# Performance work log

Hardware: AMD Instinct MI355X
Metric: run time of the kernel (lower is better)

Reference implementation:

```python
import jax, jax.numpy as jnp
import numpy as np

D = 1024
B = 16384

def setup_inputs() -> dict:
    key = jax.random.key(0)
    ks = jax.random.split(key, 8)
    s = 1.0 / np.sqrt(D)  # torch Linear default init scale (uniform), use scaled normal
    return {
        "f1": jax.random.normal(ks[0], (B, D), jnp.float32),
        "f2": jax.random.normal(ks[1], (B, D), jnp.float32),
        "Wq": jax.random.normal(ks[2], (D, D), jnp.float32) * s,
        "bq": jax.random.normal(ks[3], (D,), jnp.float32) * s,
        "Wk": jax.random.normal(ks[4], (D, D), jnp.float32) * s,
        "bk": jax.random.normal(ks[5], (D,), jnp.float32) * s,
        "Wv": jax.random.normal(ks[6], (D, D), jnp.float32) * s,
        "bv": jax.random.normal(ks[7], (D,), jnp.float32) * s,
    }

def reference(f1, f2, Wq, bq, Wk, bk, Wv, bv):
    d = f1.shape[-1]
    feats = jnp.stack([f1, f2], axis=1)          # [B, 2, D]
    # nn.Linear: y = x @ W.T + b
    Q = jnp.einsum("bsd,ed->bse", feats, Wq) + bq  # [B, 2, D]
    K = jnp.einsum("bsd,ed->bse", feats, Wk) + bk
    V = jnp.einsum("bsd,ed->bse", feats, Wv) + bv
    scores = jnp.einsum("bse,bte->bst", Q, K) / jnp.sqrt(jnp.asarray(d, feats.dtype))  # [B, 2, 2]
    attn = jax.nn.softmax(scores, axis=-1)
    attended = jnp.einsum("bst,btd->bsd", attn, V)  # [B, 2, D]
    return attended.sum(axis=1)                     # [B, D]
```

## Files before the change

kernel.cpp:

```cpp
#include <hip/hip_runtime.h>
#include <hip/hip_bf16.h>
#include <stdint.h>

typedef unsigned short u16;
typedef __bf16 bf16x8 __attribute__((ext_vector_type(8)));
typedef float f32x4 __attribute__((ext_vector_type(4)));

#define D_DIM 1024
#define B_ROWS 16384
#define M_ROWS 32768
#define BM 128
#define BN 128
#define BK 64

__device__ __forceinline__ u16 f2bs(float f) {
    union { float f; unsigned u; } v; v.f = f;
    unsigned r = v.u + 0x7FFFu + ((v.u >> 16) & 1u);
    return (u16)(r >> 16);
}
__device__ __forceinline__ float bs2f(unsigned bits16) {
    union { unsigned u; float f; } v; v.u = bits16 << 16;
    return v.f;
}
__device__ __forceinline__ float bidx(uint2 v, int e) {
    unsigned w = (e < 2) ? v.x : v.y;
    unsigned sh = (unsigned)(e & 1) * 16u;
    return bs2f((w >> sh) & 0xFFFFu);
}
__device__ __forceinline__ uint2 pack4(float4 f) {
    uint2 r;
    r.x = (unsigned)f2bs(f.x) | ((unsigned)f2bs(f.y) << 16);
    r.y = (unsigned)f2bs(f.z) | ((unsigned)f2bs(f.w) << 16);
    return r;
}

#define GLD16(gsrc, ldst)                                                      \
    __builtin_amdgcn_global_load_lds(                                          \
        (const __attribute__((address_space(1))) void*)(gsrc),                 \
        (__attribute__((address_space(3))) void*)(ldst), 16, 0, 0)

__global__ __launch_bounds__(256) void cvt_feats(const float* __restrict__ f1,
                                                 const float* __restrict__ f2,
                                                 u16* __restrict__ X) {
    size_t i4   = (size_t)blockIdx.x * 256 + threadIdx.x;
    size_t base = i4 * 4;
    size_t brow = base >> 10;
    size_t col  = base & 1023;
    float4 a = *(const float4*)(f1 + base);
    float4 b = *(const float4*)(f2 + base);
    *(uint2*)(X + (2 * brow) * D_DIM + col)     = pack4(a);
    *(uint2*)(X + (2 * brow + 1) * D_DIM + col) = pack4(b);
}

__global__ __launch_bounds__(256) void cvt_wv(const float* __restrict__ Wv,
                                              u16* __restrict__ Wvb) {
    size_t base = ((size_t)blockIdx.x * 256 + threadIdx.x) * 4;
    *(uint2*)(Wvb + base) = pack4(*(const float4*)(Wv + base));
}

__global__ __launch_bounds__(256) void transpose_bf16(const float* __restrict__ in,
                                                      u16* __restrict__ out) {
    __shared__ float lds[32][33];
    const int tx = threadIdx.x & 31;
    const int ty = threadIdx.x >> 5;
    const int r0 = (blockIdx.x >> 5) * 32;
    const int c0 = (blockIdx.x & 31) * 32;
#pragma unroll
    for (int i = 0; i < 4; ++i) {
        int r = ty + i * 8;
        lds[r][tx] = in[(size_t)(r0 + r) * D_DIM + c0 + tx];
    }
    __syncthreads();
#pragma unroll
    for (int i = 0; i < 4; ++i) {
        int r = ty + i * 8;
        out[(size_t)(c0 + r) * D_DIM + r0 + tx] = f2bs(lds[tx][r]);
    }
}

__global__ __launch_bounds__(256) void uvc_k(const float* __restrict__ Wq,
                                             const float* __restrict__ Wk,
                                             const float* __restrict__ bq,
                                             const float* __restrict__ bk,
                                             float* __restrict__ u,
                                             float* __restrict__ v,
                                             float* __restrict__ cbuf) {
    const int dl = threadIdx.x & 31;
    const int fg = threadIdx.x >> 5;
    const int d  = blockIdx.x * 32 + dl;
    float au = 0.f, av = 0.f;
    const int f0 = fg * 128;
    for (int f = f0; f < f0 + 128; ++f) {
        au = fmaf(Wq[(size_t)f * D_DIM + d], bk[f], au);
        av = fmaf(Wk[(size_t)f * D_DIM + d], bq[f], av);
    }
    __shared__ float su[8][32], sv[8][32];
    su[fg][dl] = au; sv[fg][dl] = av;
    __syncthreads();
    if (fg == 0) {
        float a = 0.f, b2 = 0.f;
#pragma unroll
        for (int g = 0; g < 8; ++g) { a += su[g][dl]; b2 += sv[g][dl]; }
        u[d] = a; v[d] = b2;
    }
    if (blockIdx.x == 0) {
        __shared__ float red[256];
        float p = 0.f;
        for (int f = threadIdx.x; f < D_DIM; f += 256) p = fmaf(bq[f], bk[f], p);
        red[threadIdx.x] = p;
        __syncthreads();
        for (int s = 128; s; s >>= 1) {
            if (threadIdx.x < s) red[threadIdx.x] += red[threadIdx.x + s];
            __syncthreads();
        }
        if (threadIdx.x == 0) cbuf[0] = red[0];
    }
}

__global__ __launch_bounds__(256, 3) void gemm_bt(const u16* __restrict__ A,
                                                  const u16* __restrict__ W,
                                                  const float* __restrict__ bias,
                                                  u16* __restrict__ C, int ncols) {
    constexpr int K = D_DIM;
    __shared__ u16 As[BM * BK];
    __shared__ u16 Bs[BN * BK];

    const int cpx  = gridDim.x >> 3;
    const int orig = (blockIdx.x & 7) * cpx + (blockIdx.x >> 3);
    const int nTn = ncols / BN;
    const int m0 = (orig / nTn) * BM, n0 = (orig % nTn) * BN;

    const int tid  = threadIdx.x;
    const int lane = tid & 63;
    const int wave = tid >> 6;
    const int wr = wave >> 1, wc = wave & 1;

    const int lr = lane & 15;
    const int kg = lane >> 4;

    f32x4 acc[4][4] = {};

    const int sr  = tid >> 3;
    const int scs = ((tid & 7) ^ ((tid >> 3) & 7)) * 8;
    const u16* aRow = A + (size_t)(m0 + sr) * K + scs;
    const u16* bRow = W + (size_t)(n0 + sr) * K + scs;
    u16* aDst = As + tid * 8;
    u16* bDst = Bs + tid * 8;

    for (int kt = 0; kt < K; kt += BK) {
#pragma unroll
        for (int i = 0; i < 4; ++i) {
            GLD16(aRow + (size_t)i * 32 * K + kt, aDst + i * 2048);
            GLD16(bRow + (size_t)i * 32 * K + kt, bDst + i * 2048);
        }
        __syncthreads();

#pragma unroll
        for (int kk = 0; kk < 2; ++kk) {
            bf16x8 af[4], bfr[4];
            const int kx = kk * 4 + kg;
#pragma unroll
            for (int mf = 0; mf < 4; ++mf) {
                const int R = wr * 64 + mf * 16 + lr;
                af[mf] = *(const bf16x8*)(As + R * 64 + ((kx ^ (R & 7)) * 8));
            }
#pragma unroll
            for (int nf = 0; nf < 4; ++nf) {
                const int S = wc * 64 + nf * 16 + lr;
                bfr[nf] = *(const bf16x8*)(Bs + S * 64 + ((kx ^ (S & 7)) * 8));
            }
#pragma unroll
            for (int mf = 0; mf < 4; ++mf)
#pragma unroll
                for (int nf = 0; nf < 4; ++nf)
                    acc[mf][nf] = __builtin_amdgcn_mfma_f32_16x16x32_bf16(
                        af[mf], bfr[nf], acc[mf][nf], 0, 0, 0);
        }
        __syncthreads();
    }

    const int cr = (lane >> 4) * 4;
    const int cc = lane & 15;
#pragma unroll
    for (int mf = 0; mf < 4; ++mf) {
#pragma unroll
        for (int nf = 0; nf < 4; ++nf) {
            int col = n0 + wc * 64 + nf * 16 + cc;
            float bsv = bias ? bias[col] : 0.f;
#pragma unroll
            for (int j = 0; j < 4; ++j) {
                int row = m0 + wr * 64 + mf * 16 + cr + j;
                C[(size_t)row * ncols + col] = f2bs(acc[mf][nf][j] + bsv);
            }
        }
    }
}

__global__ __launch_bounds__(256, 3) void gemm_cmb(const u16* __restrict__ A,
                                                   const u16* __restrict__ W,
                                                   const float* __restrict__ bias,
                                                   const float2* __restrict__ wts,
                                                   float* __restrict__ out) {
    constexpr int K = D_DIM;
    constexpr int ncols = D_DIM;
    __shared__ u16 As[BM * BK];
    __shared__ u16 Bs[BN * BK];

    const int cpx  = gridDim.x >> 3;
    const int orig = (blockIdx.x & 7) * cpx + (blockIdx.x >> 3);
    const int nTn = ncols / BN;
    const int m0 = (orig / nTn) * BM, n0 = (orig % nTn) * BN;

    const int tid  = threadIdx.x;
    const int lane = tid & 63;
    const int wave = tid >> 6;
    const int wr = wave >> 1, wc = wave & 1;

    const int lr = lane & 15;
    const int kg = lane >> 4;

    f32x4 acc[4][4] = {};

    const int sr  = tid >> 3;
    const int scs = ((tid & 7) ^ ((tid >> 3) & 7)) * 8;
    const u16* aRow = A + (size_t)(m0 + sr) * K + scs;
    const u16* bRow = W + (size_t)(n0 + sr) * K + scs;
    u16* aDst = As + tid * 8;
    u16* bDst = Bs + tid * 8;

    for (int kt = 0; kt < K; kt += BK) {
#pragma unroll
        for (int i = 0; i < 4; ++i) {
            GLD16(aRow + (size_t)i * 32 * K + kt, aDst + i * 2048);
            GLD16(bRow + (size_t)i * 32 * K + kt, bDst + i * 2048);
        }
        __syncthreads();

#pragma unroll
        for (int kk = 0; kk < 2; ++kk) {
            bf16x8 af[4], bfr[4];
            const int kx = kk * 4 + kg;
#pragma unroll
            for (int mf = 0; mf < 4; ++mf) {
                const int R = wr * 64 + mf * 16 + lr;
                af[mf] = *(const bf16x8*)(As + R * 64 + ((kx ^ (R & 7)) * 8));
            }
#pragma unroll
            for (int nf = 0; nf < 4; ++nf) {
                const int S = wc * 64 + nf * 16 + lr;
                bfr[nf] = *(const bf16x8*)(Bs + S * 64 + ((kx ^ (S & 7)) * 8));
            }
#pragma unroll
            for (int mf = 0; mf < 4; ++mf)
#pragma unroll
                for (int nf = 0; nf < 4; ++nf)
                    acc[mf][nf] = __builtin_amdgcn_mfma_f32_16x16x32_bf16(
                        af[mf], bfr[nf], acc[mf][nf], 0, 0, 0);
        }
        __syncthreads();
    }

    const int cr = (lane >> 4) * 4;
    const int cc = lane & 15;
#pragma unroll
    for (int mf = 0; mf < 4; ++mf) {
        const int rowbase = m0 + wr * 64 + mf * 16 + cr;
        const int p0 = rowbase >> 1;
        const float2 w0 = wts[p0];
        const float2 w1 = wts[p0 + 1];
#pragma unroll
        for (int nf = 0; nf < 4; ++nf) {
            int col = n0 + wc * 64 + nf * 16 + cc;
            float bsv = bias[col];
            float o0 = w0.x * (acc[mf][nf][0] + bsv) + w0.y * (acc[mf][nf][1] + bsv);
            float o1 = w1.x * (acc[mf][nf][2] + bsv) + w1.y * (acc[mf][nf][3] + bsv);
            out[(size_t)p0 * D_DIM + col]       = o0;
            out[(size_t)(p0 + 1) * D_DIM + col] = o1;
        }
    }
}

__global__ __launch_bounds__(256) void scores2(const u16* __restrict__ X,
                                               const u16* __restrict__ G,
                                               const float* __restrict__ u,
                                               const float* __restrict__ v,
                                               const float* __restrict__ cbuf,
                                               float2* __restrict__ wts) {
    const int wave = threadIdx.x >> 6;
    const int lane = threadIdx.x & 63;
    const size_t b = (size_t)blockIdx.x * 4 + wave;
    const u16* x0p = X + (2 * b) * D_DIM;
    const u16* x1p = x0p + D_DIM;
    const u16* g0p = G + (2 * b) * D_DIM;
    const u16* g1p = g0p + D_DIM;

    float d00 = 0.f, d01 = 0.f, d10 = 0.f, d11 = 0.f;
    float au0 = 0.f, au1 = 0.f, bv0 = 0.f, bv1 = 0.f;
#pragma unroll
    for (int s = 0; s < 4; ++s) {
        int c = s * 256 + lane * 4;
        uint2 x0 = *(const uint2*)(x0p + c);
        uint2 x1 = *(const uint2*)(x1p + c);
        uint2 g0 = *(const uint2*)(g0p + c);
        uint2 g1 = *(const uint2*)(g1p + c);
        float4 uu = *(const float4*)(u + c);
        float4 vv = *(const float4*)(v + c);
        float uA[4] = {uu.x, uu.y, uu.z, uu.w};
        float vA[4] = {vv.x, vv.y, vv.z, vv.w};
#pragma unroll
        for (int e = 0; e < 4; ++e) {
            float a0 = bidx(x0, e), a1 = bidx(x1, e);
            float c0 = bidx(g0, e), c1 = bidx(g1, e);
            d00 = fmaf(a0, c0, d00); d01 = fmaf(a0, c1, d01);
            d10 = fmaf(a1, c0, d10); d11 = fmaf(a1, c1, d11);
            au0 = fmaf(uA[e], a0, au0); au1 = fmaf(uA[e], a1, au1);
            bv0 = fmaf(vA[e], a0, bv0); bv1 = fmaf(vA[e], a1, bv1);
        }
    }
#pragma unroll
    for (int off = 32; off; off >>= 1) {
        d00 += __shfl_xor(d00, off); d01 += __shfl_xor(d01, off);
        d10 += __shfl_xor(d10, off); d11 += __shfl_xor(d11, off);
        au0 += __shfl_xor(au0, off); au1 += __shfl_xor(au1, off);
        bv0 += __shfl_xor(bv0, off); bv1 += __shfl_xor(bv1, off);
    }
    if (lane == 0) {
        const float cc0 = cbuf[0];
        const float sc = 1.0f / 32.0f;
        float s00 = (d00 + au0 + bv0 + cc0) * sc;
        float s01 = (d01 + au0 + bv1 + cc0) * sc;
        float s10 = (d10 + au1 + bv0 + cc0) * sc;
        float s11 = (d11 + au1 + bv1 + cc0) * sc;
        float mA = fmaxf(s00, s01);
        float e00 = expf(s00 - mA), e01 = expf(s01 - mA);
        float rA = 1.0f / (e00 + e01);
        float mB = fmaxf(s10, s11);
        float e10 = expf(s10 - mB), e11 = expf(s11 - mB);
        float rB = 1.0f / (e10 + e11);
        float2 w;
        w.x = e00 * rA + e10 * rB;
        w.y = e01 * rA + e11 * rB;
        wts[b] = w;
    }
}

extern "C" void kernel_launch(void* const* d_in, const int* in_sizes, int n_in,
                              void* d_out, int out_size, void* d_ws, size_t ws_size,
                              hipStream_t stream) {
    const float* f1 = (const float*)d_in[0];
    const float* f2 = (const float*)d_in[1];
    const float* Wq = (const float*)d_in[2];
    const float* bq = (const float*)d_in[3];
    const float* Wk = (const float*)d_in[4];
    const float* bk = (const float*)d_in[5];
    const float* Wv = (const float*)d_in[6];
    const float* bv = (const float*)d_in[7];
    float* out = (float*)d_out;

    char*   w    = (char*)d_ws;
    u16*    X    = (u16*)w;
    u16*    G    = X + (size_t)M_ROWS * D_DIM;
    u16*    Wvb  = G + (size_t)M_ROWS * D_DIM;
    u16*    WqT  = Wvb + (size_t)D_DIM * D_DIM;
    u16*    WkT  = WqT + (size_t)D_DIM * D_DIM;
    u16*    Mb   = WkT + (size_t)D_DIM * D_DIM;
    float*  u    = (float*)(Mb + (size_t)D_DIM * D_DIM);
    float*  v    = u + D_DIM;
    float*  cbuf = v + D_DIM;
    float2* wts  = (float2*)(cbuf + 64);

    cvt_feats<<<(B_ROWS * D_DIM / 4) / 256, 256, 0, stream>>>(f1, f2, X);
    cvt_wv<<<(D_DIM * D_DIM / 4) / 256, 256, 0, stream>>>(Wv, Wvb);
    transpose_bf16<<<1024, 256, 0, stream>>>(Wq, WqT);
    transpose_bf16<<<1024, 256, 0, stream>>>(Wk, WkT);
    uvc_k<<<D_DIM / 32, 256, 0, stream>>>(Wq, Wk, bq, bk, u, v, cbuf);

    gemm_bt<<<(D_DIM / BM) * (D_DIM / BN), 256, 0, stream>>>(WqT, WkT, nullptr, Mb, D_DIM);
    gemm_bt<<<(M_ROWS / BM) * (D_DIM / BN), 256, 0, stream>>>(X, Mb, nullptr, G, D_DIM);
    scores2<<<B_ROWS / 4, 256, 0, stream>>>(X, G, u, v, cbuf, wts);
    gemm_cmb<<<(M_ROWS / BM) * (D_DIM / BN), 256, 0, stream>>>(X, Wvb, bv, wts, out);
}
```

Before: 234.5 us.

## Double-buffer LDS tiles in both GEMM kernels to overlap loads with MFMA

Both GEMM kernels now keep two LDS buffers for the A and B tiles. They prefetch the next K-tile with direct global-to-LDS loads while MFMAs run on the current tile, and they drop the trailing barrier. This is meant to hide global load latency behind compute. In exchange LDS per block doubles and launch bounds fall from 3 to 2 blocks per CU, which lowers occupancy. A full vmcnt(0) wait is still taken at the top of each iteration.

```diff
diff --git a/kernel.cpp b/kernel.cpp
--- a/kernel.cpp
+++ b/kernel.cpp
@@ -117,13 +117,14 @@
     }
 }
 
-__global__ __launch_bounds__(256, 3) void gemm_bt(const u16* __restrict__ A,
+__global__ __launch_bounds__(256, 2) void gemm_bt(const u16* __restrict__ A,
                                                   const u16* __restrict__ W,
                                                   const float* __restrict__ bias,
                                                   u16* __restrict__ C, int ncols) {
     constexpr int K = D_DIM;
-    __shared__ u16 As[BM * BK];
-    __shared__ u16 Bs[BN * BK];
+    constexpr int TB = BM * BK;
+    __shared__ u16 As[2 * TB];
+    __shared__ u16 Bs[2 * TB];
 
     const int cpx  = gridDim.x >> 3;
     const int orig = (blockIdx.x & 7) * cpx + (blockIdx.x >> 3);
@@ -144,17 +145,27 @@
     const int scs = ((tid & 7) ^ ((tid >> 3) & 7)) * 8;
     const u16* aRow = A + (size_t)(m0 + sr) * K + scs;
     const u16* bRow = W + (size_t)(n0 + sr) * K + scs;
-    u16* aDst = As + tid * 8;
-    u16* bDst = Bs + tid * 8;
-
+
+#define STAGE_AB(p, kt)                                                        \
+    {                                                                          \
+        u16* aD = As + (p) * TB + tid * 8;                                     \
+        u16* bD = Bs + (p) * TB + tid * 8;                                     \
+        _Pragma("unroll")                                                      \
+        for (int i = 0; i < 4; ++i) {                                          \
+            GLD16(aRow + (size_t)i * 32 * K + (kt), aD + i * 2048);            \
+            GLD16(bRow + (size_t)i * 32 * K + (kt), bD + i * 2048);            \
+        }                                                                      \
+    }
+
+    STAGE_AB(0, 0);
+    int cur = 0;
     for (int kt = 0; kt < K; kt += BK) {
-#pragma unroll
-        for (int i = 0; i < 4; ++i) {
-            GLD16(aRow + (size_t)i * 32 * K + kt, aDst + i * 2048);
-            GLD16(bRow + (size_t)i * 32 * K + kt, bDst + i * 2048);
-        }
-        __syncthreads();
-
+        asm volatile("s_waitcnt vmcnt(0)" ::: "memory");
+        __builtin_amdgcn_s_barrier();
+        if (kt + BK < K) STAGE_AB(cur ^ 1, kt + BK);
+
+        const u16* Ab = As + cur * TB;
+        const u16* Bb = Bs + cur * TB;
 #pragma unroll
         for (int kk = 0; kk < 2; ++kk) {
             bf16x8 af[4], bfr[4];
@@ -162,12 +173,12 @@
 #pragma unroll
             for (int mf = 0; mf < 4; ++mf) {
                 const int R = wr * 64 + mf * 16 + lr;
-                af[mf] = *(const bf16x8*)(As + R * 64 + ((kx ^ (R & 7)) * 8));
+                af[mf] = *(const bf16x8*)(Ab + R * 64 + ((kx ^ (R & 7)) * 8));
             }
 #pragma unroll
             for (int nf = 0; nf < 4; ++nf) {
                 const int S = wc * 64 + nf * 16 + lr;
-                bfr[nf] = *(const bf16x8*)(Bs + S * 64 + ((kx ^ (S & 7)) * 8));
+                bfr[nf] = *(const bf16x8*)(Bb + S * 64 + ((kx ^ (S & 7)) * 8));
             }
 #pragma unroll
             for (int mf = 0; mf < 4; ++mf)
@@ -176,7 +187,7 @@
                     acc[mf][nf] = __builtin_amdgcn_mfma_f32_16x16x32_bf16(
                         af[mf], bfr[nf], acc[mf][nf], 0, 0, 0);
         }
-        __syncthreads();
+        cur ^= 1;
     }
 
     const int cr = (lane >> 4) * 4;
@@ -196,15 +207,16 @@
     }
 }
 
-__global__ __launch_bounds__(256, 3) void gemm_cmb(const u16* __restrict__ A,
+__global__ __launch_bounds__(256, 2) void gemm_cmb(const u16* __restrict__ A,
                                                    const u16* __restrict__ W,
                                                    const float* __restrict__ bias,
                                                    const float2* __restrict__ wts,
                                                    float* __restrict__ out) {
     constexpr int K = D_DIM;
     constexpr int ncols = D_DIM;
-    __shared__ u16 As[BM * BK];
-    __shared__ u16 Bs[BN * BK];
+    constexpr int TB = BM * BK;
+    __shared__ u16 As[2 * TB];
+    __shared__ u16 Bs[2 * TB];
 
     const int cpx  = gridDim.x >> 3;
     const int orig = (blockIdx.x & 7) * cpx + (blockIdx.x >> 3);
@@ -225,17 +237,16 @@
     const int scs = ((tid & 7) ^ ((tid >> 3) & 7)) * 8;
     const u16* aRow = A + (size_t)(m0 + sr) * K + scs;
     const u16* bRow = W + (size_t)(n0 + sr) * K + scs;
-    u16* aDst = As + tid * 8;
-    u16* bDst = Bs + tid * 8;
-
+
+    STAGE_AB(0, 0);
+    int cur = 0;
     for (int kt = 0; kt < K; kt += BK) {
-#pragma unroll
-        for (int i = 0; i < 4; ++i) {
-            GLD16(aRow + (size_t)i * 32 * K + kt, aDst + i * 2048);
-            GLD16(bRow + (size_t)i * 32 * K + kt, bDst + i * 2048);
-        }
-        __syncthreads();
-
+        asm volatile("s_waitcnt vmcnt(0)" ::: "memory");
+        __builtin_amdgcn_s_barrier();
+        if (kt + BK < K) STAGE_AB(cur ^ 1, kt + BK);
+
+        const u16* Ab = As + cur * TB;
+        const u16* Bb = Bs + cur * TB;
 #pragma unroll
         for (int kk = 0; kk < 2; ++kk) {
             bf16x8 af[4], bfr[4];
@@ -243,12 +254,12 @@
 #pragma unroll
             for (int mf = 0; mf < 4; ++mf) {
                 const int R = wr * 64 + mf * 16 + lr;
-                af[mf] = *(const bf16x8*)(As + R * 64 + ((kx ^ (R & 7)) * 8));
+                af[mf] = *(const bf16x8*)(Ab + R * 64 + ((kx ^ (R & 7)) * 8));
             }
 #pragma unroll
             for (int nf = 0; nf < 4; ++nf) {
                 const int S = wc * 64 + nf * 16 + lr;
-                bfr[nf] = *(const bf16x8*)(Bs + S * 64 + ((kx ^ (S & 7)) * 8));
+                bfr[nf] = *(const bf16x8*)(Bb + S * 64 + ((kx ^ (S & 7)) * 8));
             }
 #pragma unroll
             for (int mf = 0; mf < 4; ++mf)
@@ -257,7 +268,7 @@
                     acc[mf][nf] = __builtin_amdgcn_mfma_f32_16x16x32_bf16(
                         af[mf], bfr[nf], acc[mf][nf], 0, 0, 0);
         }
-        __syncthreads();
+        cur ^= 1;
     }
 
     const int cr = (lane >> 4) * 4;
```

Measured after the change: 253.7 us. 1.08x slower.

## Replace large GEMMs with 256x256 tile, 8-wave double-buffered ping-pong kernel

Applied to the files above, without the earlier changes.

The two large GEMMs (X·M and X·Wv with fused softmax-weight combine) move to a new templated kernel using 256x256 output tiles, 512 threads and a 128 KB LDS double buffer. Loads for tile t+2 are issued between MFMA phases, with s_barrier and s_setprio used to interleave LDS reads, global-to-LDS copies and MFMA clusters. The aim is more data reuse per tile and overlap of memory traffic with matrix math, replacing the non-pipelined 128x128 kernel. The cost is much higher LDS and register use (occupancy of about one block per CU) and fewer blocks in the grid.

```diff
diff --git a/kernel.cpp b/kernel.cpp
--- a/kernel.cpp
+++ b/kernel.cpp
@@ -38,6 +38,8 @@
     __builtin_amdgcn_global_load_lds(                                          \
         (const __attribute__((address_space(1))) void*)(gsrc),                 \
         (__attribute__((address_space(3))) void*)(ldst), 16, 0, 0)
+
+#define MFMA16(a, b, c) __builtin_amdgcn_mfma_f32_16x16x32_bf16((a), (b), (c), 0, 0, 0)
 
 __global__ __launch_bounds__(256) void cvt_feats(const float* __restrict__ f1,
                                                  const float* __restrict__ f2,
@@ -117,10 +119,9 @@
     }
 }
 
-__global__ __launch_bounds__(256, 3) void gemm_bt(const u16* __restrict__ A,
-                                                  const u16* __restrict__ W,
-                                                  const float* __restrict__ bias,
-                                                  u16* __restrict__ C, int ncols) {
+__global__ __launch_bounds__(256, 3) void gemm_small(const u16* __restrict__ A,
+                                                     const u16* __restrict__ W,
+                                                     u16* __restrict__ C, int ncols) {
     constexpr int K = D_DIM;
     __shared__ u16 As[BM * BK];
     __shared__ u16 Bs[BN * BK];
@@ -134,7 +135,6 @@
     const int lane = tid & 63;
     const int wave = tid >> 6;
     const int wr = wave >> 1, wc = wave & 1;
-
     const int lr = lane & 15;
     const int kg = lane >> 4;
 
@@ -154,7 +154,6 @@
             GLD16(bRow + (size_t)i * 32 * K + kt, bDst + i * 2048);
         }
         __syncthreads();
-
 #pragma unroll
         for (int kk = 0; kk < 2; ++kk) {
             bf16x8 af[4], bfr[4];
@@ -173,8 +172,7 @@
             for (int mf = 0; mf < 4; ++mf)
 #pragma unroll
                 for (int nf = 0; nf < 4; ++nf)
-                    acc[mf][nf] = __builtin_amdgcn_mfma_f32_16x16x32_bf16(
-                        af[mf], bfr[nf], acc[mf][nf], 0, 0, 0);
+                    acc[mf][nf] = MFMA16(af[mf], bfr[nf], acc[mf][nf]);
         }
         __syncthreads();
     }
@@ -182,100 +180,196 @@
     const int cr = (lane >> 4) * 4;
     const int cc = lane & 15;
 #pragma unroll
-    for (int mf = 0; mf < 4; ++mf) {
+    for (int mf = 0; mf < 4; ++mf)
 #pragma unroll
         for (int nf = 0; nf < 4; ++nf) {
             int col = n0 + wc * 64 + nf * 16 + cc;
-            float bsv = bias ? bias[col] : 0.f;
 #pragma unroll
             for (int j = 0; j < 4; ++j) {
                 int row = m0 + wr * 64 + mf * 16 + cr + j;
-                C[(size_t)row * ncols + col] = f2bs(acc[mf][nf][j] + bsv);
-            }
-        }
-    }
-}
-
-__global__ __launch_bounds__(256, 3) void gemm_cmb(const u16* __restrict__ A,
-                                                   const u16* __restrict__ W,
-                                                   const float* __restrict__ bias,
-                                                   const float2* __restrict__ wts,
-                                                   float* __restrict__ out) {
-    constexpr int K = D_DIM;
-    constexpr int ncols = D_DIM;
-    __shared__ u16 As[BM * BK];
-    __shared__ u16 Bs[BN * BK];
+                C[(size_t)row * ncols + col] = f2bs(acc[mf][nf][j]);
+            }
+        }
+}
+
+template<bool FUSED>
+__global__ __launch_bounds__(512, 2) void gemm8p(const u16* __restrict__ A,
+                                                 const u16* __restrict__ W,
+                                                 const float* __restrict__ bias,
+                                                 u16* __restrict__ C,
+                                                 const float2* __restrict__ wts,
+                                                 float* __restrict__ out,
+                                                 int ncols) {
+    constexpr int K  = D_DIM;
+    constexpr int NT = K / 64;
+    __shared__ u16 L[65536];
 
     const int cpx  = gridDim.x >> 3;
     const int orig = (blockIdx.x & 7) * cpx + (blockIdx.x >> 3);
-    const int nTn = ncols / BN;
-    const int m0 = (orig / nTn) * BM, n0 = (orig % nTn) * BN;
+    const int nTn  = ncols >> 8;
+    const int m0 = (orig / nTn) << 8, n0 = (orig % nTn) << 8;
 
     const int tid  = threadIdx.x;
     const int lane = tid & 63;
-    const int wave = tid >> 6;
-    const int wr = wave >> 1, wc = wave & 1;
-
+    const int wid  = tid >> 6;
+    const int wm = wid >> 2, wn = wid & 3;
     const int lr = lane & 15;
     const int kg = lane >> 4;
-
-    f32x4 acc[4][4] = {};
-
-    const int sr  = tid >> 3;
-    const int scs = ((tid & 7) ^ ((tid >> 3) & 7)) * 8;
-    const u16* aRow = A + (size_t)(m0 + sr) * K + scs;
-    const u16* bRow = W + (size_t)(n0 + sr) * K + scs;
-    u16* aDst = As + tid * 8;
-    u16* bDst = Bs + tid * 8;
-
-    for (int kt = 0; kt < K; kt += BK) {
-#pragma unroll
-        for (int i = 0; i < 4; ++i) {
-            GLD16(aRow + (size_t)i * 32 * K + kt, aDst + i * 2048);
-            GLD16(bRow + (size_t)i * 32 * K + kt, bDst + i * 2048);
-        }
-        __syncthreads();
-
-#pragma unroll
-        for (int kk = 0; kk < 2; ++kk) {
-            bf16x8 af[4], bfr[4];
-            const int kx = kk * 4 + kg;
-#pragma unroll
-            for (int mf = 0; mf < 4; ++mf) {
-                const int R = wr * 64 + mf * 16 + lr;
-                af[mf] = *(const bf16x8*)(As + R * 64 + ((kx ^ (R & 7)) * 8));
-            }
-#pragma unroll
-            for (int nf = 0; nf < 4; ++nf) {
-                const int S = wc * 64 + nf * 16 + lr;
-                bfr[nf] = *(const bf16x8*)(Bs + S * 64 + ((kx ^ (S & 7)) * 8));
-            }
-#pragma unroll
-            for (int mf = 0; mf < 4; ++mf)
-#pragma unroll
-                for (int nf = 0; nf < 4; ++nf)
-                    acc[mf][nf] = __builtin_amdgcn_mfma_f32_16x16x32_bf16(
-                        af[mf], bfr[nf], acc[mf][nf], 0, 0, 0);
-        }
-        __syncthreads();
-    }
+    const int r7 = lr & 7;
+    const int cx0 = ((0 + kg) ^ r7) * 8;
+    const int cx1 = ((4 + kg) ^ r7) * 8;
+    const int sS  = (wn & 1) * 64;
+
+    const int rb  = tid >> 3;
+    const int scs = ((tid & 7) ^ (rb & 7)) * 8;
+    const u16* aB = A + (size_t)(m0 + rb) * K + scs;
+    const u16* bB = W + (size_t)(n0 + rb) * K + scs;
+    u16* aD = L + tid * 8;
+    u16* bD = L + 32768 + tid * 8;
+
+#define ST_HALF(tile, h)                                                       \
+    {                                                                          \
+        const int d_ = (tile) & 1;                                             \
+        const size_t ko_ = (size_t)(tile) * 64;                                \
+        if ((h) < 2) {                                                         \
+            const u16* s_ = aB + (size_t)(h) * 128 * K + ko_;                  \
+            u16* t_ = aD + (d_ * 2 + (h)) * 8192;                              \
+            GLD16(s_, t_);                                                     \
+            GLD16(s_ + (size_t)64 * K, t_ + 4096);                            \
+        } else {                                                               \
+            const u16* s_ = bB + (size_t)((h) - 2) * 128 * K + ko_;            \
+            u16* t_ = bD + (d_ * 2 + ((h) - 2)) * 8192;                        \
+            GLD16(s_, t_);                                                     \
+            GLD16(s_ + (size_t)64 * K, t_ + 4096);                            \
+        }                                                                      \
+    }
+
+    f32x4 acc[8][4] = {};
+    bf16x8 af[8][2], bf[4][2];
+
+#pragma unroll
+    for (int h = 0; h < 4; ++h) ST_HALF(0, h);
+#pragma unroll
+    for (int h = 0; h < 4; ++h) ST_HALF(1, h);
+    asm volatile("s_waitcnt vmcnt(8)" ::: "memory");
+    __builtin_amdgcn_s_barrier();
+
+#pragma unroll 2
+    for (int t = 0; t < NT; ++t) {
+        const int d = t & 1;
+        const u16* Ab = L + (d * 2 + wm) * 8192;
+        const u16* Bb = L + 32768 + (d * 2 + (wn >> 1)) * 8192;
+        const bool more = (t + 2 < NT);
+
+#pragma unroll
+        for (int m = 0; m < 4; ++m) {
+            const int R = m * 16 + lr;
+            af[m][0] = *(const bf16x8*)(Ab + R * 64 + cx0);
+            af[m][1] = *(const bf16x8*)(Ab + R * 64 + cx1);
+        }
+#pragma unroll
+        for (int n = 0; n < 2; ++n) {
+            const int S = sS + n * 16 + lr;
+            bf[n][0] = *(const bf16x8*)(Bb + S * 64 + cx0);
+            bf[n][1] = *(const bf16x8*)(Bb + S * 64 + cx1);
+        }
+        __builtin_amdgcn_s_barrier();
+        __builtin_amdgcn_s_setprio(1);
+#pragma unroll
+        for (int m = 0; m < 4; ++m)
+#pragma unroll
+            for (int n = 0; n < 2; ++n) {
+                acc[m][n] = MFMA16(af[m][0], bf[n][0], acc[m][n]);
+                acc[m][n] = MFMA16(af[m][1], bf[n][1], acc[m][n]);
+            }
+        __builtin_amdgcn_s_setprio(0);
+        __builtin_amdgcn_s_barrier();
+
+#pragma unroll
+        for (int n = 2; n < 4; ++n) {
+            const int S = sS + n * 16 + lr;
+            bf[n][0] = *(const bf16x8*)(Bb + S * 64 + cx0);
+            bf[n][1] = *(const bf16x8*)(Bb + S * 64 + cx1);
+        }
+        __builtin_amdgcn_s_barrier();
+        __builtin_amdgcn_s_setprio(1);
+#pragma unroll
+        for (int m = 0; m < 4; ++m)
+#pragma unroll
+            for (int n = 2; n < 4; ++n) {
+                acc[m][n] = MFMA16(af[m][0], bf[n][0], acc[m][n]);
+                acc[m][n] = MFMA16(af[m][1], bf[n][1], acc[m][n]);
+            }
+        __builtin_amdgcn_s_setprio(0);
+        __builtin_amdgcn_s_barrier();
+
+#pragma unroll
+        for (int m = 4; m < 8; ++m) {
+            const int R = m * 16 + lr;
+            af[m][0] = *(const bf16x8*)(Ab + R * 64 + cx0);
+            af[m][1] = *(const bf16x8*)(Ab + R * 64 + cx1);
+        }
+        if (more) { ST_HALF(t + 2, 2); ST_HALF(t + 2, 3); }
+        __builtin_amdgcn_s_barrier();
+        __builtin_amdgcn_s_setprio(1);
+#pragma unroll
+        for (int m = 4; m < 8; ++m)
+#pragma unroll
+            for (int n = 0; n < 2; ++n) {
+                acc[m][n] = MFMA16(af[m][0], bf[n][0], acc[m][n]);
+                acc[m][n] = MFMA16(af[m][1], bf[n][1], acc[m][n]);
+            }
+        __builtin_amdgcn_s_setprio(0);
+        __builtin_amdgcn_s_barrier();
+
+        if (more) { ST_HALF(t + 2, 0); ST_HALF(t + 2, 1); }
+        __builtin_amdgcn_s_barrier();
+        __builtin_amdgcn_s_setprio(1);
+#pragma unroll
+        for (int m = 4; m < 8; ++m)
+#pragma unroll
+            for (int n = 2; n < 4; ++n) {
+                acc[m][n] = MFMA16(af[m][0], bf[n][0], acc[m][n]);
+                acc[m][n] = MFMA16(af[m][1], bf[n][1], acc[m][n]);
+            }
+        __builtin_amdgcn_s_setprio(0);
+        if (more) asm volatile("s_waitcnt vmcnt(8)" ::: "memory");
+        else      asm volatile("s_waitcnt vmcnt(0)" ::: "memory");
+        __builtin_amdgcn_s_barrier();
+    }
+#undef ST_HALF
 
     const int cr = (lane >> 4) * 4;
     const int cc = lane & 15;
-#pragma unroll
-    for (int mf = 0; mf < 4; ++mf) {
-        const int rowbase = m0 + wr * 64 + mf * 16 + cr;
-        const int p0 = rowbase >> 1;
-        const float2 w0 = wts[p0];
-        const float2 w1 = wts[p0 + 1];
-#pragma unroll
-        for (int nf = 0; nf < 4; ++nf) {
-            int col = n0 + wc * 64 + nf * 16 + cc;
-            float bsv = bias[col];
-            float o0 = w0.x * (acc[mf][nf][0] + bsv) + w0.y * (acc[mf][nf][1] + bsv);
-            float o1 = w1.x * (acc[mf][nf][2] + bsv) + w1.y * (acc[mf][nf][3] + bsv);
-            out[(size_t)p0 * D_DIM + col]       = o0;
-            out[(size_t)(p0 + 1) * D_DIM + col] = o1;
+    if constexpr (!FUSED) {
+#pragma unroll
+        for (int mf = 0; mf < 8; ++mf)
+#pragma unroll
+            for (int nf = 0; nf < 4; ++nf) {
+                int col = n0 + wn * 64 + nf * 16 + cc;
+                float bsv = bias ? bias[col] : 0.f;
+#pragma unroll
+                for (int j = 0; j < 4; ++j) {
+                    int row = m0 + wm * 128 + mf * 16 + cr + j;
+                    C[(size_t)row * ncols + col] = f2bs(acc[mf][nf][j] + bsv);
+                }
+            }
+    } else {
+#pragma unroll
+        for (int mf = 0; mf < 8; ++mf) {
+            const int rowbase = m0 + wm * 128 + mf * 16 + cr;
+            const int p0 = rowbase >> 1;
+            const float2 w0 = wts[p0];
+            const float2 w1 = wts[p0 + 1];
+#pragma unroll
+            for (int nf = 0; nf < 4; ++nf) {
+                int col = n0 + wn * 64 + nf * 16 + cc;
+                float bsv = bias[col];
+                float o0 = w0.x * (acc[mf][nf][0] + bsv) + w0.y * (acc[mf][nf][1] + bsv);
+                float o1 = w1.x * (acc[mf][nf][2] + bsv) + w1.y * (acc[mf][nf][3] + bsv);
+                out[(size_t)p0 * D_DIM + col]       = o0;
+                out[(size_t)(p0 + 1) * D_DIM + col] = o1;
+            }
         }
     }
 }
@@ -375,8 +469,10 @@
     transpose_bf16<<<1024, 256, 0, stream>>>(Wk, WkT);
     uvc_k<<<D_DIM / 32, 256, 0, stream>>>(Wq, Wk, bq, bk, u, v, cbuf);
 
-    gemm_bt<<<(D_DIM / BM) * (D_DIM / BN), 256, 0, stream>>>(WqT, WkT, nullptr, Mb, D_DIM);
-    gemm_bt<<<(M_ROWS / BM) * (D_DIM / BN), 256, 0, stream>>>(X, Mb, nullptr, G, D_DIM);
+    gemm_small<<<(D_DIM / BM) * (D_DIM / BN), 256, 0, stream>>>(WqT, WkT, Mb, D_DIM);
+    gemm8p<false><<<(M_ROWS / 256) * (D_DIM / 256), 512, 0, stream>>>(
+        X, Mb, nullptr, G, nullptr, nullptr, D_DIM);
     scores2<<<B_ROWS / 4, 256, 0, stream>>>(X, G, u, v, cbuf, wts);
-    gemm_cmb<<<(M_ROWS / BM) * (D_DIM / BN), 256, 0, stream>>>(X, Wvb, bv, wts, out);
-}
+    gemm8p<true><<<(M_ROWS / 256) * (D_DIM / 256), 512, 0, stream>>>(
+        X, Wvb, bv, nullptr, wts, out, D_DIM);
+}
```

New measurement: 227.3 us. -3.1%, faster.
